# Kernel tuning notes

Hardware: AMD Instinct MI355X
Metric: run time of the kernel (lower is better)

## Reference

```python
import jax, jax.numpy as jnp
import numpy as np
from jax import lax

K = 3          # kernel_size
PAD = 1
D = 2 * K - 2  # 4 trajectory directions
C_IN = 64
C_OUT = 128


def setup_inputs() -> dict:
    key = jax.random.key(0)
    k1, k2, k3, k4, k5 = jax.random.split(key, 5)
    N, C, H, W = 4, C_IN, 128, 128
    x = jax.random.normal(k1, (N, C, H, W), dtype=jnp.float32)
    # conv_offset: Conv2d(C, 2*K*K, K, pad=1, bias=True)
    w_off = jax.random.normal(k2, (2 * K * K, C, K, K), dtype=jnp.float32) * (1.0 / np.sqrt(C * K * K)) * 0.1
    b_off = jax.random.normal(k3, (2 * K * K,), dtype=jnp.float32) * 0.1
    # conv1: DeformConv2d(C, C*D, K, pad=1, groups=C) -> weight (C*D, 1, K, K)
    w_deform = jax.random.normal(k4, (C * D, 1, K, K), dtype=jnp.float32) * (1.0 / np.sqrt(K * K))
    # conv2: 1x1 conv (C*D -> C_OUT), no bias
    w_pw = jax.random.normal(k5, (C_OUT, C * D), dtype=jnp.float32) * (1.0 / np.sqrt(C * D))
    return {"x": x, "w_off": w_off, "b_off": b_off, "w_deform": w_deform, "w_pw": w_pw}


def _deform_sample(x, offsets):
    """Bilinear-sample x at K*K learned-offset locations per output pixel.
    x: (N,C,H,W); offsets: (N, 2*K*K, H, W) with (dy,dx) pairs per kernel tap.
    Returns (N, C, K*K, H, W)."""
    N, C, H, W = x.shape
    kk = K * K
    off = offsets.reshape(N, kk, 2, H, W)
    dy, dx = off[:, :, 0], off[:, :, 1]                    # (N,kk,H,W)
    ky = jnp.repeat(jnp.arange(K), K).astype(jnp.float32)  # (kk,)
    kx = jnp.tile(jnp.arange(K), K).astype(jnp.float32)
    base_y = (jnp.arange(H, dtype=jnp.float32)[None, :, None] - PAD + ky[:, None, None])  # (kk,H,1)
    base_x = (jnp.arange(W, dtype=jnp.float32)[None, None, :] - PAD + kx[:, None, None])  # (kk,1,W)
    py = dy + base_y[None]
    px = dx + base_x[None]
    y0 = jnp.floor(py)
    x0 = jnp.floor(px)
    wy = (py - y0)[:, None]   # (N,1,kk,H,W)
    wx = (px - x0)[:, None]
    y0i = y0.astype(jnp.int32)
    x0i = x0.astype(jnp.int32)
    xf = x.reshape(N, C, H * W)

    def gather(yi, xi):
        valid = ((yi >= 0) & (yi < H) & (xi >= 0) & (xi < W)).astype(x.dtype)
        idx = jnp.clip(yi, 0, H - 1) * W + jnp.clip(xi, 0, W - 1)   # (N,kk,H,W)
        vals = jax.vmap(lambda xn, idxn: xn[:, idxn])(xf, idx)       # (N,C,kk,H,W)
        return vals * valid[:, None]

    v00 = gather(y0i, x0i)
    v01 = gather(y0i, x0i + 1)
    v10 = gather(y0i + 1, x0i)
    v11 = gather(y0i + 1, x0i + 1)
    return (v00 * (1 - wy) * (1 - wx) + v01 * (1 - wy) * wx
            + v10 * wy * (1 - wx) + v11 * wy * wx)


def reference(x, w_off, b_off, w_deform, w_pw):
    N, C, H, W = x.shape
    # conv_offset (3x3, pad 1)
    t = lax.conv_general_dilated(x, w_off, (1, 1), [(PAD, PAD), (PAD, PAD)],
                                 dimension_numbers=("NCHW", "OIHW", "NCHW"))
    t = t + b_off[None, :, None, None]
    # diff_conv with conv_offset: subtract 1x1 conv of x with spatially-summed weight
    ws_off = w_off.sum((2, 3))                               # (2KK, C)
    t = t - jnp.einsum("nchw,oc->nohw", x, ws_off)
    # depthwise deformable conv: sample then contract over kernel taps
    samp = _deform_sample(x, t)                               # (N,C,KK,H,W)
    wd = w_deform.reshape(C, D, K * K)
    y = jnp.einsum("ncphw,cdp->ncdhw", samp, wd).reshape(N, C * D, H, W)
    # diff_conv with conv1 (grouped 1x1: each input channel scales its D outputs)
    ws_d = w_deform.sum((2, 3)).reshape(C, D)
    y = y - jnp.einsum("nchw,cd->ncdhw", x, ws_d).reshape(N, C * D, H, W)
    # pointwise conv2
    return jnp.einsum("nchw,oc->nohw", y, w_pw)
```

## Files before the change

### kernel.cpp

```cpp
#include <hip/hip_runtime.h>

#define DDIM   4
#define CIN    64
#define COUT   128
#define CDIM   256
#define HH     128
#define WWID   128
#define NN     4
#define KK     9
#define OFFC   18
#define HW     (HH * WWID)

#define XS_SLICE  438
#define XS_TOTAL  (8 * XS_SLICE)
#define TL_OFF    XS_TOTAL
#define YL_OFF    (TL_OFF + OFFC * 64)
#define SMEM_FLOATS (YL_OFF + 8192)

typedef __attribute__((ext_vector_type(8))) short bf16x8;
typedef __attribute__((ext_vector_type(4))) float f32x4;

#define RFL(x) __builtin_amdgcn_readfirstlane(x)

__device__ __forceinline__ unsigned short f2bf(float f) {
  union { float f; unsigned u; } c; c.f = f;
  unsigned u = c.u;
  return (unsigned short)((u + 0x7FFFu + ((u >> 16) & 1u)) >> 16);
}
__device__ __forceinline__ float bf2f(unsigned short u) {
  union { unsigned u; float f; } c; c.u = (unsigned)u << 16;
  return c.f;
}

__global__ void convert_wpw(const float* __restrict__ w_pw, unsigned short* __restrict__ wbf) {
  int i = blockIdx.x * 256 + threadIdx.x;
  if (i < COUT * CDIM) wbf[i] = f2bf(w_pw[i]);
}

__global__ __launch_bounds__(512, 2)
void fused_all(const float* __restrict__ x, const float* __restrict__ w_off,
               const float* __restrict__ b_off, const float* __restrict__ w_deform,
               const unsigned short* __restrict__ wbf, float* __restrict__ out) {
  __shared__ float smem[SMEM_FLOATS];

  const int lin = blockIdx.x + 2 * blockIdx.y + 256 * blockIdx.z;
  const int swz = ((lin & 7) << 7) + (lin >> 3);
  const int n  = swz >> 8;
  const int h  = (swz >> 1) & 127;
  const int w0 = (swz & 1) * 64;

  const int tid = threadIdx.x;
  const int pl = tid & 63;
  const int cg = tid >> 6;
  const int w = w0 + pl;
  const int pix = h * WWID + w;

  const float* xn = x + (size_t)n * CIN * HW;
  float* xsl = smem + cg * XS_SLICE;
  float* tl  = smem + TL_OFF;
  unsigned short* pt   = (unsigned short*)(smem + YL_OFF);
  unsigned short* ylds = (unsigned short*)(smem + YL_OFF);

  float ao[OFFC];
#pragma unroll
  for (int o = 0; o < OFFC; ++o) ao[o] = 0.f;

#pragma unroll 1
  for (int ci = 0; ci < 8; ++ci) {
    const int c = RFL(cg * 8 + ci);
    const float* xc = xn + (size_t)c * HW;
    for (int i = pl; i < 198; i += 64) {
      const int tr = i / 66, tc = i - tr * 66;
      const int gy = h - 1 + tr, gx = w0 - 1 + tc;
      float v = 0.f;
      if (gy >= 0 && gy < HH && gx >= 0 && gx < WWID) v = xc[gy * WWID + gx];
      xsl[tr * 66 + tc] = v;
    }
    const float center = xsl[66 + pl + 1];
    float v[KK];
#pragma unroll
    for (int p = 0; p < KK; ++p)
      v[p] = xsl[(p / 3) * 66 + pl + (p % 3)] - center;
#pragma unroll
    for (int o = 0; o < OFFC; ++o) {
      const float* wrow = w_off + ((size_t)o * CIN + c) * KK;
      float a = ao[o];
#pragma unroll
      for (int p = 0; p < KK; ++p) {
        if (p == 4) continue;
        a += wrow[p] * v[p];
      }
      ao[o] = a;
    }
  }
#pragma unroll
  for (int o = 0; o < OFFC; ++o) pt[(cg * OFFC + o) * 64 + pl] = f2bf(ao[o]);
  __syncthreads();

  for (int idx = tid; idx < OFFC * 64; idx += 512) {
    const int o = idx >> 6, px = idx & 63;
    float s = b_off[o];
#pragma unroll
    for (int w8 = 0; w8 < 8; ++w8) s += bf2f(pt[(w8 * OFFC + o) * 64 + px]);
    tl[o * 64 + px] = s;
  }
  __syncthreads();

  const int row0 = h - 3;
  const int col0 = w0 - 3;
  float c00[KK], c01[KK], c10[KK], c11[KK];
  int gbase[KK];
  unsigned hotm = 0;
#pragma unroll
  for (int p = 0; p < KK; ++p) {
    const float dy = tl[(2 * p) * 64 + pl];
    const float dx = tl[(2 * p + 1) * 64 + pl];
    const float py  = dy + (float)(h + p / 3 - 1);
    const float pxx = dx + (float)(w + p % 3 - 1);
    const float fy = floorf(py), fx = floorf(pxx);
    const int y0 = (int)fy, x0 = (int)fx;
    const float ay = py - fy, ax = pxx - fx;
    const int ty0 = y0 - row0;
    const int tx0 = x0 - col0;
    if ((unsigned)ty0 <= 4u && (unsigned)tx0 <= 70u) hotm |= 1u << p;
    gbase[p] = ty0 * 73 + tx0;
    const float by = 1.f - ay, bx = 1.f - ax;
    c00[p] = by * bx;  c01[p] = by * ax;
    c10[p] = ay * bx;  c11[p] = ay * ax;
  }
  const bool hot = (__all((int)(hotm == 0x1FFu)) != 0);

  int g1[7], l1[7];
  unsigned ok7 = 0;
#pragma unroll
  for (int k = 0; k < 7; ++k) {
    const int i = pl + k * 64;
    const int r = i / 72, cl = i - r * 72;
    const int gy = row0 + r, gx = col0 + cl;
    const bool act = (i < 432) && gy >= 0 && gy < HH && gx >= 0 && gx < WWID;
    g1[k] = act ? (gy * WWID + gx) : 0;
    l1[k] = r * 73 + cl;
    if (act) ok7 |= 1u << k;
  }
  auto p1_load = [&](float* b, int c) {
    const float* xc = xn + (size_t)c * HW;
#pragma unroll
    for (int k = 0; k < 7; ++k)
      b[k] = ((ok7 >> k) & 1) ? xc[g1[k]] : 0.f;
  };
  auto p1_write = [&](const float* b) {
#pragma unroll
    for (int k = 0; k < 7; ++k) {
      if (k < 6) xsl[l1[k]] = b[k];
      else if (pl < 48) xsl[l1[6]] = b[6];
    }
  };
  auto store_y = [&](int c, float yd0, float yd1, float yd2, float yd3) {
    const unsigned lo = (unsigned)f2bf(yd0) | ((unsigned)f2bf(yd1) << 16);
    const unsigned hi = (unsigned)f2bf(yd2) | ((unsigned)f2bf(yd3) << 16);
    const int ebase = (((c >> 1) ^ (pl & 7)) << 3) + (c & 1) * 4;
    *reinterpret_cast<uint2*>(&ylds[pl * CDIM + ebase]) = make_uint2(lo, hi);
  };

  auto p1_comp_hot = [&](int c) {
    const float xcv = xsl[3 * 73 + pl + 3];
    float g00[KK], g01[KK], g10[KK], g11[KK];
#pragma unroll
    for (int p = 0; p < KK; ++p) {
      const float* bp = &xsl[gbase[p]];
      g00[p] = bp[0];  g01[p] = bp[1];
      g10[p] = bp[73]; g11[p] = bp[74];
    }
    float yd0 = 0.f, yd1 = 0.f, yd2 = 0.f, yd3 = 0.f;
#pragma unroll
    for (int p = 0; p < KK; ++p) {
      const float samp = c00[p] * g00[p] + c01[p] * g01[p]
                       + c10[p] * g10[p] + c11[p] * g11[p];
      const float s = samp - xcv;
      const float* wdp = w_deform + (size_t)(c * DDIM) * KK + p;
      yd0 += wdp[0 * KK] * s;
      yd1 += wdp[1 * KK] * s;
      yd2 += wdp[2 * KK] * s;
      yd3 += wdp[3 * KK] * s;
    }
    store_y(c, yd0, yd1, yd2, yd3);
  };

  auto p1_comp_cold = [&](int c) {
    const float* xc = xn + (size_t)c * HW;
    const float xcv = xc[pix];
    float yd0 = 0.f, yd1 = 0.f, yd2 = 0.f, yd3 = 0.f;
#pragma unroll
    for (int p = 0; p < KK; ++p) {
      float samp;
      if (hotm & (1u << p)) {
        const float* bp = &xsl[gbase[p]];
        samp = c00[p] * bp[0] + c01[p] * bp[1] + c10[p] * bp[73] + c11[p] * bp[74];
      } else {
        const float dy = tl[(2 * p) * 64 + pl];
        const float dx = tl[(2 * p + 1) * 64 + pl];
        const float py  = dy + (float)(h + p / 3 - 1);
        const float pxx = dx + (float)(w + p % 3 - 1);
        const float fy = floorf(py), fx = floorf(pxx);
        const int y0 = (int)fy, x0 = (int)fx;
        const int y1 = y0 + 1,  x1 = x0 + 1;
        const bool vy0 = (y0 >= 0) && (y0 < HH), vy1 = (y1 >= 0) && (y1 < HH);
        const bool vx0 = (x0 >= 0) && (x0 < WWID), vx1 = (x1 >= 0) && (x1 < WWID);
        const int yc0 = min(max(y0, 0), HH - 1),  yc1 = min(max(y1, 0), HH - 1);
        const int xc0 = min(max(x0, 0), WWID - 1), xc1 = min(max(x1, 0), WWID - 1);
        const float m00 = (vy0 && vx0) ? c00[p] : 0.f;
        const float m01 = (vy0 && vx1) ? c01[p] : 0.f;
        const float m10 = (vy1 && vx0) ? c10[p] : 0.f;
        const float m11 = (vy1 && vx1) ? c11[p] : 0.f;
        samp = m00 * xc[yc0 * WWID + xc0] + m01 * xc[yc0 * WWID + xc1]
             + m10 * xc[yc1 * WWID + xc0] + m11 * xc[yc1 * WWID + xc1];
      }
      const float s = samp - xcv;
      const float* wdp = w_deform + (size_t)(c * DDIM) * KK + p;
      yd0 += wdp[0 * KK] * s;
      yd1 += wdp[1 * KK] * s;
      yd2 += wdp[2 * KK] * s;
      yd3 += wdp[3 * KK] * s;
    }
    store_y(c, yd0, yd1, yd2, yd3);
  };

  auto pipeline = [&](auto comp) {
    float qA[7], qB[7];
    p1_load(qA, RFL(cg * 8));
#pragma unroll
    for (int c2 = 0; c2 < 8; c2 += 2) {
      p1_write(qA);
      p1_load(qB, RFL(cg * 8 + c2 + 1));
      comp(RFL(cg * 8 + c2));
      p1_write(qB);
      if (c2 < 6) p1_load(qA, RFL(cg * 8 + c2 + 2));
      comp(RFL(cg * 8 + c2 + 1));
    }
  };
  if (hot) pipeline(p1_comp_hot);
  else     pipeline(p1_comp_cold);
  __syncthreads();

  const int l15 = tid & 15;
  const int kg  = (tid & 63) >> 4;
  const int Mb = (cg >> 1) * 32;
  const int Nb = (cg & 1) * 32;

  f32x4 acc[2][2];
#pragma unroll
  for (int mi = 0; mi < 2; ++mi)
#pragma unroll
    for (int ni = 0; ni < 2; ++ni)
      acc[mi][ni] = (f32x4){0.f, 0.f, 0.f, 0.f};

#pragma unroll
  for (int ks = 0; ks < 8; ++ks) {
    bf16x8 bfr[2];
#pragma unroll
    for (int ni = 0; ni < 2; ++ni) {
      const int prow = Nb + ni * 16 + l15;
      const int chunk = ks * 4 + kg;
      const int eb = ((chunk ^ (prow & 7)) << 3);
      bfr[ni] = *reinterpret_cast<const bf16x8*>(&ylds[prow * CDIM + eb]);
    }
    bf16x8 afr[2];
#pragma unroll
    for (int mi = 0; mi < 2; ++mi) {
      const int o = Mb + mi * 16 + l15;
      afr[mi] = *reinterpret_cast<const bf16x8*>(wbf + (size_t)o * CDIM + ks * 32 + kg * 8);
    }
#pragma unroll
    for (int mi = 0; mi < 2; ++mi)
#pragma unroll
      for (int ni = 0; ni < 2; ++ni)
        acc[mi][ni] = __builtin_amdgcn_mfma_f32_16x16x32_bf16(afr[mi], bfr[ni], acc[mi][ni], 0, 0, 0);
  }

  float* on = out + (size_t)n * COUT * HW;
#pragma unroll
  for (int mi = 0; mi < 2; ++mi) {
#pragma unroll
    for (int ni = 0; ni < 2; ++ni) {
      const int pcol = h * WWID + w0 + Nb + ni * 16 + l15;
#pragma unroll
      for (int reg = 0; reg < 4; ++reg) {
        const int o = Mb + mi * 16 + kg * 4 + reg;
        on[(size_t)o * HW + pcol] = acc[mi][ni][reg];
      }
    }
  }
}

extern "C" void kernel_launch(void* const* d_in, const int* in_sizes, int n_in,
                              void* d_out, int out_size, void* d_ws, size_t ws_size,
                              hipStream_t stream) {
  const float* x        = (const float*)d_in[0];
  const float* w_off    = (const float*)d_in[1];
  const float* b_off    = (const float*)d_in[2];
  const float* w_deform = (const float*)d_in[3];
  const float* w_pw     = (const float*)d_in[4];
  float* out = (float*)d_out;
  unsigned short* wbf = (unsigned short*)d_ws;

  convert_wpw<<<dim3(COUT * CDIM / 256), dim3(256), 0, stream>>>(w_pw, wbf);
  fused_all<<<dim3(WWID / 64, HH, NN), dim3(512), 0, stream>>>(x, w_off, b_off, w_deform, wbf, out);
}
```

Baseline: 152.1 us.

## Double-buffer offset-conv halo loads, store offsets as bf16, reswizzle Y LDS

The offset-convolution stage now precomputes its halo gather indices and software-pipelines the global loads for the next channel into registers while the current channel is computed, which hides global load latency. The reduced offset tile is stored in LDS as bf16 rather than fp32, halving that region. The LDS swizzle for the bf16 Y tile gains a row-dependent rotation to spread bank accesses further. Rounding the offsets to bf16 lowers the precision of the sampling positions and may affect accuracy, and the extra prefetch buffers add register pressure.

```diff
diff --git a/kernel.cpp b/kernel.cpp
--- a/kernel.cpp
+++ b/kernel.cpp
@@ -14,7 +14,7 @@
 #define XS_SLICE  438
 #define XS_TOTAL  (8 * XS_SLICE)
 #define TL_OFF    XS_TOTAL
-#define YL_OFF    (TL_OFF + OFFC * 64)
+#define YL_OFF    (TL_OFF + 576)
 #define SMEM_FLOATS (YL_OFF + 8192)
 
 typedef __attribute__((ext_vector_type(8))) short bf16x8;
@@ -57,7 +57,7 @@
 
   const float* xn = x + (size_t)n * CIN * HW;
   float* xsl = smem + cg * XS_SLICE;
-  float* tl  = smem + TL_OFF;
+  unsigned short* tlb  = (unsigned short*)(smem + TL_OFF);
   unsigned short* pt   = (unsigned short*)(smem + YL_OFF);
   unsigned short* ylds = (unsigned short*)(smem + YL_OFF);
 
@@ -65,17 +65,30 @@
 #pragma unroll
   for (int o = 0; o < OFFC; ++o) ao[o] = 0.f;
 
-#pragma unroll 1
-  for (int ci = 0; ci < 8; ++ci) {
-    const int c = RFL(cg * 8 + ci);
+  int g0[4], l0[4]; unsigned okm = 0;
+#pragma unroll
+  for (int k = 0; k < 4; ++k) {
+    const int i = pl + k * 64;
+    const int tr = i / 66, tc = i - tr * 66;
+    const int gy = h - 1 + tr, gx = w0 - 1 + tc;
+    const bool ok = (i < 198) && gy >= 0 && gy < HH && gx >= 0 && gx < WWID;
+    g0[k] = ok ? (gy * WWID + gx) : 0;
+    l0[k] = tr * 66 + tc;
+    okm |= ok ? (1u << k) : 0u;
+  }
+  auto p0_load = [&](float* b, int c) {
     const float* xc = xn + (size_t)c * HW;
-    for (int i = pl; i < 198; i += 64) {
-      const int tr = i / 66, tc = i - tr * 66;
-      const int gy = h - 1 + tr, gx = w0 - 1 + tc;
-      float v = 0.f;
-      if (gy >= 0 && gy < HH && gx >= 0 && gx < WWID) v = xc[gy * WWID + gx];
-      xsl[tr * 66 + tc] = v;
-    }
+#pragma unroll
+    for (int k = 0; k < 4; ++k) b[k] = ((okm >> k) & 1) ? xc[g0[k]] : 0.f;
+  };
+  auto p0_write = [&](const float* b) {
+#pragma unroll
+    for (int k = 0; k < 4; ++k) {
+      if (k < 3) xsl[l0[k]] = b[k];
+      else if (pl < 6) xsl[l0[3]] = b[3];
+    }
+  };
+  auto p0_comp = [&](int c) {
     const float center = xsl[66 + pl + 1];
     float v[KK];
 #pragma unroll
@@ -92,6 +105,20 @@
       }
       ao[o] = a;
     }
+  };
+
+  {
+    float pA[4], pB[4];
+    p0_load(pA, RFL(cg * 8));
+#pragma unroll
+    for (int c2 = 0; c2 < 8; c2 += 2) {
+      p0_write(pA);
+      p0_load(pB, RFL(cg * 8 + c2 + 1));
+      p0_comp(RFL(cg * 8 + c2));
+      p0_write(pB);
+      if (c2 < 6) p0_load(pA, RFL(cg * 8 + c2 + 2));
+      p0_comp(RFL(cg * 8 + c2 + 1));
+    }
   }
 #pragma unroll
   for (int o = 0; o < OFFC; ++o) pt[(cg * OFFC + o) * 64 + pl] = f2bf(ao[o]);
@@ -102,7 +129,7 @@
     float s = b_off[o];
 #pragma unroll
     for (int w8 = 0; w8 < 8; ++w8) s += bf2f(pt[(w8 * OFFC + o) * 64 + px]);
-    tl[o * 64 + px] = s;
+    tlb[o * 64 + px] = f2bf(s);
   }
   __syncthreads();
 
@@ -113,8 +140,8 @@
   unsigned hotm = 0;
 #pragma unroll
   for (int p = 0; p < KK; ++p) {
-    const float dy = tl[(2 * p) * 64 + pl];
-    const float dx = tl[(2 * p + 1) * 64 + pl];
+    const float dy = bf2f(tlb[(2 * p) * 64 + pl]);
+    const float dx = bf2f(tlb[(2 * p + 1) * 64 + pl]);
     const float py  = dy + (float)(h + p / 3 - 1);
     const float pxx = dx + (float)(w + p % 3 - 1);
     const float fy = floorf(py), fx = floorf(pxx);
@@ -158,8 +185,9 @@
   auto store_y = [&](int c, float yd0, float yd1, float yd2, float yd3) {
     const unsigned lo = (unsigned)f2bf(yd0) | ((unsigned)f2bf(yd1) << 16);
     const unsigned hi = (unsigned)f2bf(yd2) | ((unsigned)f2bf(yd3) << 16);
-    const int ebase = (((c >> 1) ^ (pl & 7)) << 3) + (c & 1) * 4;
-    *reinterpret_cast<uint2*>(&ylds[pl * CDIM + ebase]) = make_uint2(lo, hi);
+    const int m = c >> 1;
+    const int phys = ((m ^ (pl & 7)) + (pl >> 3)) & 31;
+    *reinterpret_cast<uint2*>(&ylds[pl * CDIM + phys * 8 + (c & 1) * 4]) = make_uint2(lo, hi);
   };
 
   auto p1_comp_hot = [&](int c) {
@@ -197,8 +225,8 @@
         const float* bp = &xsl[gbase[p]];
         samp = c00[p] * bp[0] + c01[p] * bp[1] + c10[p] * bp[73] + c11[p] * bp[74];
       } else {
-        const float dy = tl[(2 * p) * 64 + pl];
-        const float dx = tl[(2 * p + 1) * 64 + pl];
+        const float dy = bf2f(tlb[(2 * p) * 64 + pl]);
+        const float dx = bf2f(tlb[(2 * p + 1) * 64 + pl]);
         const float py  = dy + (float)(h + p / 3 - 1);
         const float pxx = dx + (float)(w + p % 3 - 1);
         const float fy = floorf(py), fx = floorf(pxx);
@@ -260,9 +288,9 @@
 #pragma unroll
     for (int ni = 0; ni < 2; ++ni) {
       const int prow = Nb + ni * 16 + l15;
-      const int chunk = ks * 4 + kg;
-      const int eb = ((chunk ^ (prow & 7)) << 3);
-      bfr[ni] = *reinterpret_cast<const bf16x8*>(&ylds[prow * CDIM + eb]);
+      const int m = ks * 4 + kg;
+      const int phys = ((m ^ (prow & 7)) + (prow >> 3)) & 31;
+      bfr[ni] = *reinterpret_cast<const bf16x8*>(&ylds[prow * CDIM + phys * 8]);
     }
     bf16x8 afr[2];
 #pragma unroll
```

New measurement: 224.9 us. +47.9%, slower.
